# Performance work log

Hardware: AMD Instinct MI355X
Metric: run time of the kernel (lower is better)

The kernel has to match this reference:

```python
import jax, jax.numpy as jnp
import numpy as np


def _conv_nchw(x, w, strides):
    # F.conv2d with padding=0 -> VALID, NCHW / OIHW layout
    return jax.lax.conv_general_dilated(
        x, w, window_strides=tuple(strides), padding="VALID",
        dimension_numbers=("NCHW", "OIHW", "NCHW"))


def setup_inputs() -> dict:
    key = jax.random.key(0)
    kx, kw, kb = jax.random.split(key, 3)
    # scale so values span the full int8 range and all 8 bit-planes are active
    x = jax.random.normal(kx, (64, 64, 56, 56), dtype=jnp.float32) * 60.0
    weight = jax.random.normal(kw, (128, 64, 3, 3), dtype=jnp.float32) * 0.05
    bias = jax.random.normal(kb, (128,), dtype=jnp.float32)
    return {"x": x, "weight": weight, "bias": bias}


def reference(x, weight, bias):
    strides = (1, 1)
    # clamp to int8 range and cast (torch.clamp + .type(torch.int8))
    xi = jnp.clip(x, -128, 127).astype(jnp.int8)
    y = jnp.zeros((), dtype=weight.dtype)
    for i in range(8):
        # arithmetic shift on signed int8, matching torch semantics
        bit = ((xi >> i) & 1).astype(weight.dtype)
        yi = jnp.clip(_conv_nchw(bit, weight, strides), -1024, 1023)
        scale = jnp.asarray(-128.0 if i == 7 else float(2 ** i), dtype=weight.dtype)
        y = y + yi * scale
    y = y + bias.reshape(1, -1, 1, 1)
    return y
```

## Files before the change

### kernel.cpp

```cpp
#include <hip/hip_runtime.h>
#include <stdint.h>

typedef unsigned short u16;
typedef unsigned int u32;
typedef __attribute__((ext_vector_type(8))) __bf16 bf16x8;
typedef __attribute__((ext_vector_type(4))) float f32x4;

#define N_IMG 64
#define C_IN  64
#define HW_IN 3136
#define W_IN  56
#define C_OUT 128
#define OH    54
#define OW    54
#define SPI   2916
#define KTOT  576
#define M_TOTAL (N_IMG*SPI)

typedef __attribute__((address_space(3))) unsigned int lds_uint;
typedef __attribute__((address_space(1))) unsigned int gbl_uint;

__device__ __forceinline__ void load16_to_lds(const u16* g, u16* l) {
  __builtin_amdgcn_global_load_lds((const gbl_uint*)g, (lds_uint*)l, 16, 0, 0);
}

__device__ inline u16 f32_bf16_rne(float f) {
  unsigned u = __float_as_uint(f);
  u = (u + 0x7FFFu + ((u >> 16) & 1u)) >> 16;
  return (u16)u;
}

__global__ __launch_bounds__(256) void convert_xw(const float* __restrict__ x,
                                                  const float* __restrict__ w,
                                                  u16* __restrict__ xt,
                                                  u16* __restrict__ wtT) {
  if (blockIdx.x == 49) {
    int o = blockIdx.y * 256 + threadIdx.x;
    #pragma unroll
    for (int it = 0; it < 5; it++) {
      int oo = o + it * 16384;
      if (oo < C_OUT * KTOT) {
        int co = oo / KTOT;
        int k  = oo - co * KTOT;
        int t2 = k >> 6, ci = k & 63;
        wtT[oo] = f32_bf16_rne(w[co * KTOT + ci * 9 + t2]);
      }
    }
    return;
  }
  __shared__ u16 tile[64][65];
  int t  = threadIdx.x;
  int tx = t & 63, ty = t >> 6;
  int n  = blockIdx.y;
  int s0 = blockIdx.x * 64;
  const float* xp = x + (size_t)n * C_IN * HW_IN + s0;
  #pragma unroll
  for (int i = ty; i < 64; i += 4) {
    float v = xp[i * HW_IN + tx];
    v = fminf(fmaxf(v, -128.f), 127.f);
    v = truncf(v);
    tile[i][tx] = (u16)(__float_as_uint(v) >> 16);
  }
  __syncthreads();
  u32* op = (u32*)(xt + (size_t)n * HW_IN * C_IN) + (size_t)s0 * 32;
  #pragma unroll
  for (int j = 0; j < 8; j++) {
    int sp = j * 8 + ty * 2 + (tx >> 5);
    int cp = tx & 31;
    u32 lo = tile[2 * cp][sp];
    u32 hi = tile[2 * cp + 1][sp];
    op[sp * 32 + cp] = lo | (hi << 16);
  }
}

__global__ __launch_bounds__(256) void conv_gemm(
    const u16* __restrict__ xt, const u16* __restrict__ wtT,
    const float* __restrict__ bias, float* __restrict__ y)
{
  __shared__ u16 sP[2][8192];
  __shared__ u16 sW[2][8192];

  int tid  = threadIdx.x;
  int wv   = tid >> 6;
  int lane = tid & 63;
  int ln   = lane & 15;
  int q    = lane >> 4;
  int wy   = wv >> 1;
  int wx   = wv & 1;

  int blk_sp0 = blockIdx.x * 128;

  int r8 = lane >> 3;
  int cg = lane & 7;
  int scol = (cg ^ r8) * 8;

  int pix_off[4], wt_off[4];
  #pragma unroll
  for (int j = 0; j < 4; j++) {
    int srow = wv * 32 + j * 8 + r8;
    int p   = blk_sp0 + srow;
    int img = p / SPI;  int rem = p - img * SPI;
    int oh  = rem / OW; int ow  = rem - oh * OW;
    pix_off[j] = (img * HW_IN + oh * W_IN + ow) * C_IN + scol;
    wt_off[j]  = srow * KTOT + scol;
  }

  f32x4 acc[4][4];
  #pragma unroll
  for (int mt = 0; mt < 4; mt++)
    #pragma unroll
    for (int nt = 0; nt < 4; nt++)
      acc[mt][nt] = (f32x4){0.f, 0.f, 0.f, 0.f};

  int wrow[4], prow[4];
  #pragma unroll
  for (int i = 0; i < 4; i++) {
    wrow[i] = (wy * 64 + i * 16 + ln) * 64;
    prow[i] = (wx * 64 + i * 16 + ln) * 64;
  }
  int l7 = ln & 7;

#define STAGE(KC, BUF) do {                                                   \
    int xoff_ = (((KC) / 3) * W_IN + ((KC) % 3)) * C_IN;                      \
    _Pragma("unroll")                                                         \
    for (int j_ = 0; j_ < 4; j_++)                                            \
      load16_to_lds(xt + pix_off[j_] + xoff_,                                 \
                    &sP[BUF][(wv * 32 + j_ * 8) * 64]);                       \
    _Pragma("unroll")                                                         \
    for (int j_ = 0; j_ < 4; j_++)                                            \
      load16_to_lds(wtT + wt_off[j_] + (KC) * 64,                             \
                    &sW[BUF][(wv * 32 + j_ * 8) * 64]);                       \
  } while (0)

  STAGE(0, 0);

  #pragma unroll
  for (int kc = 0; kc < 9; kc++) {
    int rb = kc & 1;
    __syncthreads();
    if (kc < 8) STAGE(kc + 1, rb ^ 1);

    #pragma unroll
    for (int s = 0; s < 2; s++) {
      int pg = ((s * 4 + q) ^ l7) * 8;
      bf16x8 wf[4], pf[4];
      #pragma unroll
      for (int mt = 0; mt < 4; mt++)
        wf[mt] = *(const bf16x8*)(&sW[rb][0] + wrow[mt] + pg);
      #pragma unroll
      for (int nt = 0; nt < 4; nt++)
        pf[nt] = *(const bf16x8*)(&sP[rb][0] + prow[nt] + pg);
      #pragma unroll
      for (int mt = 0; mt < 4; mt++)
        #pragma unroll
        for (int nt = 0; nt < 4; nt++)
          acc[mt][nt] = __builtin_amdgcn_mfma_f32_16x16x32_bf16(
              wf[mt], pf[nt], acc[mt][nt], 0, 0, 0);
    }
  }
#undef STAGE

  __syncthreads();
  float* wbuf = ((float*)sP) + wv * (16 * 66);
  int p   = blk_sp0 + wx * 64 + lane;
  int img = p / SPI;  int rem = p - img * SPI;
  size_t ybase = (size_t)img * C_OUT * SPI + rem;

  #pragma unroll
  for (int mt = 0; mt < 4; mt++) {
    #pragma unroll
    for (int nt = 0; nt < 4; nt++)
      #pragma unroll
      for (int r = 0; r < 4; r++)
        wbuf[(q * 4 + r) * 66 + nt * 16 + ln] = acc[mt][nt][r];
    int co0 = wy * 64 + mt * 16;
    #pragma unroll
    for (int c = 0; c < 16; c++) {
      float v = wbuf[c * 66 + lane] + bias[co0 + c];
      y[ybase + (size_t)(co0 + c) * SPI] = v;
    }
  }
}

extern "C" void kernel_launch(void* const* d_in, const int* in_sizes, int n_in,
                              void* d_out, int out_size, void* d_ws, size_t ws_size,
                              hipStream_t stream) {
  const float* x    = (const float*)d_in[0];
  const float* w    = (const float*)d_in[1];
  const float* bias = (const float*)d_in[2];
  float* y = (float*)d_out;

  u16* wtT = (u16*)d_ws;
  u16* xt  = (u16*)((char*)d_ws + (size_t)C_OUT * KTOT * sizeof(u16));

  hipLaunchKernelGGL(convert_xw, dim3(50, 64), dim3(256), 0, stream, x, w, xt, wtT);
  hipLaunchKernelGGL(conv_gemm, dim3(M_TOTAL / 128), dim3(256), 0, stream,
                     xt, wtT, bias, y);
}
```

Before: 194.4 us.

## Tile conv by output rows with LDS-resident input halo and direct weight loads

Restructures the implicit GEMM so each block handles two output rows of one image and loads the four needed input rows into LDS once, reusing them across all nine filter taps instead of re-staging pixels per tap. Weights are read directly from global memory per tap, removing the double-buffered LDS staging and per-tap barriers. The epilogue writes contiguous output rows per channel. This trades some wasted MFMA work (54-wide rows padded to 64) and global-latency weight loads for far less input traffic and higher occupancy.

```diff
diff --git a/kernel.cpp b/kernel.cpp
--- a/kernel.cpp
+++ b/kernel.cpp
@@ -15,7 +15,6 @@
 #define OW    54
 #define SPI   2916
 #define KTOT  576
-#define M_TOTAL (N_IMG*SPI)
 
 typedef __attribute__((address_space(3))) unsigned int lds_uint;
 typedef __attribute__((address_space(1))) unsigned int gbl_uint;
@@ -73,12 +72,11 @@
   }
 }
 
-__global__ __launch_bounds__(256) void conv_gemm(
+__global__ __launch_bounds__(256, 3) void conv_gemm(
     const u16* __restrict__ xt, const u16* __restrict__ wtT,
     const float* __restrict__ bias, float* __restrict__ y)
 {
-  __shared__ u16 sP[2][8192];
-  __shared__ u16 sW[2][8192];
+  __shared__ alignas(16) u16 lds[15104];
 
   int tid  = threadIdx.x;
   int wv   = tid >> 6;
@@ -88,22 +86,33 @@
   int wy   = wv >> 1;
   int wx   = wv & 1;
 
-  int blk_sp0 = blockIdx.x * 128;
+  int n   = blockIdx.y;
+  int oh0 = blockIdx.x * 2;
 
-  int r8 = lane >> 3;
-  int cg = lane & 7;
-  int scol = (cg ^ r8) * 8;
+  {
+    const u16* src = xt + ((size_t)n * HW_IN + (size_t)(oh0 + wv) * W_IN) * C_IN;
+    u16* dst = lds + wv * (W_IN * C_IN);
+    #pragma unroll
+    for (int it = 0; it < 7; it++) {
+      int gidx = it * 64 + lane;
+      int col  = gidx >> 3, gs = gidx & 7;
+      int sgrp = col * 8 + (gs ^ (col & 7));
+      load16_to_lds(src + sgrp * 8, dst + it * 512);
+    }
+  }
 
-  int pix_off[4], wt_off[4];
+  int wbase[4];
   #pragma unroll
-  for (int j = 0; j < 4; j++) {
-    int srow = wv * 32 + j * 8 + r8;
-    int p   = blk_sp0 + srow;
-    int img = p / SPI;  int rem = p - img * SPI;
-    int oh  = rem / OW; int ow  = rem - oh * OW;
-    pix_off[j] = (img * HW_IN + oh * W_IN + ow) * C_IN + scol;
-    wt_off[j]  = srow * KTOT + scol;
-  }
+  for (int mt = 0; mt < 4; mt++)
+    wbase[mt] = (wy * 64 + mt * 16 + ln) * KTOT + q * 8;
+
+  int poff[3][2];
+  #pragma unroll
+  for (int kw = 0; kw < 3; kw++)
+    #pragma unroll
+    for (int s = 0; s < 2; s++)
+      poff[kw][s] = (wx * W_IN + ln + kw) * 128
+                  + (((s * 4 + q) ^ ((ln + kw) & 7)) * 16);
 
   f32x4 acc[4][4];
   #pragma unroll
@@ -112,44 +121,21 @@
     for (int nt = 0; nt < 4; nt++)
       acc[mt][nt] = (f32x4){0.f, 0.f, 0.f, 0.f};
 
-  int wrow[4], prow[4];
+  __syncthreads();
+
+  const char* ldsb = (const char*)lds;
   #pragma unroll
-  for (int i = 0; i < 4; i++) {
-    wrow[i] = (wy * 64 + i * 16 + ln) * 64;
-    prow[i] = (wx * 64 + i * 16 + ln) * 64;
-  }
-  int l7 = ln & 7;
-
-#define STAGE(KC, BUF) do {                                                   \
-    int xoff_ = (((KC) / 3) * W_IN + ((KC) % 3)) * C_IN;                      \
-    _Pragma("unroll")                                                         \
-    for (int j_ = 0; j_ < 4; j_++)                                            \
-      load16_to_lds(xt + pix_off[j_] + xoff_,                                 \
-                    &sP[BUF][(wv * 32 + j_ * 8) * 64]);                       \
-    _Pragma("unroll")                                                         \
-    for (int j_ = 0; j_ < 4; j_++)                                            \
-      load16_to_lds(wtT + wt_off[j_] + (KC) * 64,                             \
-                    &sW[BUF][(wv * 32 + j_ * 8) * 64]);                       \
-  } while (0)
-
-  STAGE(0, 0);
-
-  #pragma unroll
-  for (int kc = 0; kc < 9; kc++) {
-    int rb = kc & 1;
-    __syncthreads();
-    if (kc < 8) STAGE(kc + 1, rb ^ 1);
-
+  for (int tap = 0; tap < 9; tap++) {
+    const int kh = tap / 3, kw = tap - kh * 3;
     #pragma unroll
     for (int s = 0; s < 2; s++) {
-      int pg = ((s * 4 + q) ^ l7) * 8;
       bf16x8 wf[4], pf[4];
       #pragma unroll
       for (int mt = 0; mt < 4; mt++)
-        wf[mt] = *(const bf16x8*)(&sW[rb][0] + wrow[mt] + pg);
+        wf[mt] = *(const bf16x8*)(wtT + wbase[mt] + tap * 64 + s * 32);
       #pragma unroll
       for (int nt = 0; nt < 4; nt++)
-        pf[nt] = *(const bf16x8*)(&sP[rb][0] + prow[nt] + pg);
+        pf[nt] = *(const bf16x8*)(ldsb + poff[kw][s] + kh * 7168 + nt * 2048);
       #pragma unroll
       for (int mt = 0; mt < 4; mt++)
         #pragma unroll
@@ -158,26 +144,38 @@
               wf[mt], pf[nt], acc[mt][nt], 0, 0, 0);
     }
   }
-#undef STAGE
 
-  __syncthreads();
-  float* wbuf = ((float*)sP) + wv * (16 * 66);
-  int p   = blk_sp0 + wx * 64 + lane;
-  int img = p / SPI;  int rem = p - img * SPI;
-  size_t ybase = (size_t)img * C_OUT * SPI + rem;
+  float* wbuf = (float*)lds;
+  size_t ybase_blk = (size_t)n * C_OUT * SPI + (size_t)oh0 * OW;
 
   #pragma unroll
-  for (int mt = 0; mt < 4; mt++) {
+  for (int phase = 0; phase < 2; phase++) {
+    __syncthreads();
+    if (wy == phase) {
+      #pragma unroll
+      for (int mt = 0; mt < 4; mt++)
+        #pragma unroll
+        for (int nt = 0; nt < 4; nt++) {
+          int ow = nt * 16 + ln;
+          if (ow < OW) {
+            #pragma unroll
+            for (int r = 0; r < 4; r++)
+              wbuf[(mt * 16 + q * 4 + r) * 108 + wx * OW + ow] = acc[mt][nt][r];
+          }
+        }
+    }
+    __syncthreads();
     #pragma unroll
-    for (int nt = 0; nt < 4; nt++)
+    for (int i = 0; i < 16; i++) {
+      int col = wv * 16 + i;
+      int cog = phase * 64 + col;
+      float b = bias[cog];
+      size_t yb = ybase_blk + (size_t)cog * SPI;
       #pragma unroll
-      for (int r = 0; r < 4; r++)
-        wbuf[(q * 4 + r) * 66 + nt * 16 + ln] = acc[mt][nt][r];
-    int co0 = wy * 64 + mt * 16;
-    #pragma unroll
-    for (int c = 0; c < 16; c++) {
-      float v = wbuf[c * 66 + lane] + bias[co0 + c];
-      y[ybase + (size_t)(co0 + c) * SPI] = v;
+      for (int it = 0; it < 2; it++) {
+        int idx = it * 64 + lane;
+        if (idx < 108) y[yb + idx] = wbuf[col * 108 + idx] + b;
+      }
     }
   }
 }
@@ -194,6 +192,6 @@
   u16* xt  = (u16*)((char*)d_ws + (size_t)C_OUT * KTOT * sizeof(u16));
 
   hipLaunchKernelGGL(convert_xw, dim3(50, 64), dim3(256), 0, stream, x, w, xt, wtT);
-  hipLaunchKernelGGL(conv_gemm, dim3(M_TOTAL / 128), dim3(256), 0, stream,
+  hipLaunchKernelGGL(conv_gemm, dim3(OH / 2, N_IMG), dim3(256), 0, stream,
                      xt, wtT, bias, y);
 }
```

Result: slower. 226.1 us (+16.3%).
